# Kernel tuning notes

Hardware: AMD Instinct MI355X
Metric: run time of the kernel (lower is better)

Reference implementation:

```python
import jax, jax.numpy as jnp
import numpy as np

N_NODES = 50000
N_EDGES = 800000
D_FEAT = 96
HIDDEN = 96
AVG_DEG = 16.0


def setup_inputs() -> dict:
    key = jax.random.key(0)
    k1, k2, k3, k4, k5 = jax.random.split(key, 5)
    x = jax.random.normal(k1, (N_NODES, D_FEAT), dtype=jnp.float32)
    row = jax.random.randint(k2, (N_EDGES,), 0, N_NODES)
    col = jax.random.randint(k3, (N_EDGES,), 0, N_NODES)
    edge_index = jnp.stack([row, col]).astype(jnp.int32)  # [2, E]
    # normalized adjacency values ~ 1/degree scale
    edge_weight = jax.random.uniform(k4, (N_EDGES,), dtype=jnp.float32) / AVG_DEG
    # init_w: small normal + identity (random=False path)
    W = 0.1 * jax.random.normal(k5, (D_FEAT, HIDDEN), dtype=jnp.float32) + jnp.eye(D_FEAT, HIDDEN, dtype=jnp.float32)
    b = jnp.zeros((HIDDEN,), dtype=jnp.float32)
    return {"x": x, "W": W, "b": b, "edge_index": edge_index, "edge_weight": edge_weight}


def reference(x, W, b, edge_index, edge_weight):
    # dense projection + bias
    h = x @ W + b  # [N, H]
    # sparse adj matmul: out[i] = sum_e w_e * h[col_e] for row_e == i
    row, col = edge_index[0], edge_index[1]
    msgs = edge_weight[:, None] * h[col]  # [E, H]
    pre_nonlinearity = jax.ops.segment_sum(msgs, row, num_segments=N_NODES)  # [N, H]
    # inference path: no dropout (training=None)
    output = jax.nn.elu(pre_nonlinearity)
    return (pre_nonlinearity, output)
```

## Files before the change

### kernel.cpp

```cpp
#include <hip/hip_runtime.h>


#define D 96
#define BSHIFT 5
#define BROWS 32
#define CAP 768
#define CPAD 16
#define EB_CHUNK 3200
#define NBKT_MAX 1600
#define GR 64
#define NFRAG 18

typedef unsigned long long u64;
typedef unsigned short u16;
typedef unsigned int u32;

typedef __attribute__((ext_vector_type(8))) __bf16 bf8_t;
typedef __attribute__((ext_vector_type(8))) short s8_t;
typedef __attribute__((ext_vector_type(4))) float f4_t;

__device__ __forceinline__ u16 f2bf(float f) {
  const u32 u = __float_as_uint(f);
  return (u16)((u + 0x7FFFu + ((u >> 16) & 1u)) >> 16);
}
__device__ __forceinline__ float bf2f(u16 s) {
  return __uint_as_float(((u32)s) << 16);
}

__device__ __forceinline__ f4_t mfma16(s8_t a, s8_t b, f4_t c) {
  return __builtin_amdgcn_mfma_f32_16x16x32_bf16(
      __builtin_bit_cast(bf8_t, a), __builtin_bit_cast(bf8_t, b), c, 0, 0, 0);
}

__global__ __launch_bounds__(256) void setup_kernel(
    const float* __restrict__ W, u16* __restrict__ whi, u16* __restrict__ wlo,
    int* __restrict__ bcur, int nbkt) {
  const int i = blockIdx.x * 256 + threadIdx.x;
  if (i < nbkt) bcur[i * CPAD] = 0;
  if (i < NFRAG * 64) {
    const int f = i >> 6;
    const int lane = i & 63;
    const int n = f / 3, kt = f - 3 * n;
    const int g = lane >> 4, l15 = lane & 15;
    const int col = n * 16 + l15;
#pragma unroll
    for (int j = 0; j < 8; ++j) {
      const float w = W[(kt * 32 + 8 * g + j) * D + col];
      const u16 hb = f2bf(w);
      whi[(size_t)(f * 64 + lane) * 8 + j] = hb;
      wlo[(size_t)(f * 64 + lane) * 8 + j] = f2bf(w - bf2f(hb));
    }
  }
}

struct BzSmem {
  int cnt[NBKT_MAX];
  int cur[NBKT_MAX];
  int rbuf[EB_CHUNK];
};

__global__ __launch_bounds__(256, 6) void fused_gemm_bucketize(
    const float* __restrict__ x, const u16* __restrict__ whi,
    const u16* __restrict__ wlo, const float* __restrict__ bias,
    u16* __restrict__ h16, int n_nodes,
    const int* __restrict__ rows, const int* __restrict__ cols,
    const float* __restrict__ ew, int* __restrict__ bcur,
    u64* __restrict__ tmp, int n_edges, int nbkt, int bb) {
  __shared__ BzSmem sm;
  const int tid = threadIdx.x;

  if ((int)blockIdx.x < bb) {
    for (int i = tid; i < NBKT_MAX; i += 256) sm.cnt[i] = 0;
    __syncthreads();
    const int e0 = blockIdx.x * EB_CHUNK;
    const int e1 = min(e0 + EB_CHUNK, n_edges);
    for (int e = e0 + tid; e < e1; e += 256) {
      const int r = rows[e];
      sm.rbuf[e - e0] = r;
      atomicAdd(&sm.cnt[r >> BSHIFT], 1);
    }
    __syncthreads();
    for (int b = tid; b < nbkt; b += 256) {
      const int c = sm.cnt[b];
      sm.cur[b] = (c > 0) ? atomicAdd(&bcur[b * CPAD], c) : 0;
    }
    __syncthreads();
    for (int e = e0 + tid; e < e1; e += 256) {
      const int r = sm.rbuf[e - e0];
      const int b = r >> BSHIFT;
      const u64 u = ((u64)__float_as_uint(ew[e]) << 32) |
                    ((u64)(r & (BROWS - 1)) << 20) | (u64)(unsigned)cols[e];
      const int pos = atomicAdd(&sm.cur[b], 1);
      if (pos < CAP) tmp[(size_t)b * CAP + pos] = u;
    }
  } else {
    const int wid = tid >> 6;
    const int lane = tid & 63;
    const int l15 = lane & 15;
    const int g = lane >> 4;
    const int row0 = ((int)blockIdx.x - bb) * GR + wid * 16;

    const int ra = min(row0 + l15, n_nodes - 1);
    const float* xr = x + (size_t)ra * D;
    s8_t ah[3], al[3];
#pragma unroll
    for (int kt = 0; kt < 3; ++kt) {
      const float4 v0 = *(const float4*)(xr + kt * 32 + 8 * g);
      const float4 v1 = *(const float4*)(xr + kt * 32 + 8 * g + 4);
      const float vv[8] = {v0.x, v0.y, v0.z, v0.w, v1.x, v1.y, v1.z, v1.w};
#pragma unroll
      for (int j = 0; j < 8; ++j) {
        const u16 hb = f2bf(vv[j]);
        ah[kt][j] = (short)hb;
        al[kt][j] = (short)f2bf(vv[j] - bf2f(hb));
      }
    }

    f4_t acc[6];
#pragma unroll
    for (int n = 0; n < 6; ++n) {
      const float bv = bias[n * 16 + l15];
      acc[n][0] = bv; acc[n][1] = bv; acc[n][2] = bv; acc[n][3] = bv;
    }

#pragma unroll
    for (int kt = 0; kt < 3; ++kt) {
#pragma unroll
      for (int n = 0; n < 6; ++n) {
        const int f = n * 3 + kt;
        const s8_t bh = *(const s8_t*)(whi + (size_t)(f * 64 + lane) * 8);
        const s8_t bl = *(const s8_t*)(wlo + (size_t)(f * 64 + lane) * 8);
        acc[n] = mfma16(ah[kt], bh, acc[n]);
        acc[n] = mfma16(al[kt], bh, acc[n]);
        acc[n] = mfma16(ah[kt], bl, acc[n]);
      }
    }

#pragma unroll
    for (int n = 0; n < 6; ++n) {
#pragma unroll
      for (int r = 0; r < 4; ++r) {
        const int row = row0 + 4 * g + r;
        if (row < n_nodes)
          h16[(size_t)row * D + n * 16 + l15] = f2bf(acc[n][r]);
      }
    }
  }
}

__global__ __launch_bounds__(256) void bucket_gather_kernel(
    const int* __restrict__ bcur, const u64* __restrict__ tmp,
    const u16* __restrict__ h16, float* __restrict__ pre,
    float* __restrict__ out, int n_nodes) {
  __shared__ u64 raw[CAP];
  __shared__ u64 se[CAP];
  __shared__ int cnt[BROWS];
  __shared__ int off[BROWS + 1];
  __shared__ int cur[BROWS];
  const int tid = threadIdx.x;
  const int b = blockIdx.x;
  if (tid < BROWS) cnt[tid] = 0;
  __syncthreads();

  const int base = b * CAP;
  int count = bcur[b * CPAD];
  if (count > CAP) count = CAP;

  for (int k = tid; k < count; k += 256) {
    const u64 u = tmp[base + k];
    raw[k] = u;
    atomicAdd(&cnt[(int)((u >> 20) & (BROWS - 1))], 1);
  }
  __syncthreads();

  if (tid < BROWS) off[tid + 1] = cnt[tid];
  if (tid == 0) off[0] = 0;
  __syncthreads();
  for (int d = 1; d <= BROWS; d <<= 1) {
    int v = 0;
    if (tid <= BROWS && tid >= d) v = off[tid - d];
    __syncthreads();
    if (tid <= BROWS) off[tid] += v;
    __syncthreads();
  }
  if (tid < BROWS) cur[tid] = off[tid];
  __syncthreads();

  for (int k = tid; k < count; k += 256) {
    const u64 u = raw[k];
    const int rl = (int)((u >> 20) & (BROWS - 1));
    se[atomicAdd(&cur[rl], 1)] = u;
  }
  __syncthreads();

  const int g = tid >> 5;
  const int lane = tid & 31;
  const int row0 = b * BROWS;
#pragma unroll
  for (int j = 0; j < 4; ++j) {
    const int r = g * 4 + j;
    const int row = row0 + r;
    const int s = off[r], e = off[r + 1];
    float a0 = 0.f, a1 = 0.f, a2 = 0.f;
    int k = s;
    for (; k + 3 < e; k += 4) {
      const u64 u0 = se[k], u1 = se[k + 1], u2 = se[k + 2], u3 = se[k + 3];
      const u16* h0 = h16 + (size_t)(u0 & 0xFFFFF) * D;
      const u16* h1 = h16 + (size_t)(u1 & 0xFFFFF) * D;
      const u16* h2 = h16 + (size_t)(u2 & 0xFFFFF) * D;
      const u16* h3 = h16 + (size_t)(u3 & 0xFFFFF) * D;
      const float w0 = __uint_as_float((u32)(u0 >> 32));
      const float w1 = __uint_as_float((u32)(u1 >> 32));
      const float w2 = __uint_as_float((u32)(u2 >> 32));
      const float w3 = __uint_as_float((u32)(u3 >> 32));
      const float p00 = bf2f(h0[lane]), p01 = bf2f(h0[lane + 32]), p02 = bf2f(h0[lane + 64]);
      const float p10 = bf2f(h1[lane]), p11 = bf2f(h1[lane + 32]), p12 = bf2f(h1[lane + 64]);
      const float p20 = bf2f(h2[lane]), p21 = bf2f(h2[lane + 32]), p22 = bf2f(h2[lane + 64]);
      const float p30 = bf2f(h3[lane]), p31 = bf2f(h3[lane + 32]), p32 = bf2f(h3[lane + 64]);
      a0 = fmaf(w0, p00, a0); a1 = fmaf(w0, p01, a1); a2 = fmaf(w0, p02, a2);
      a0 = fmaf(w1, p10, a0); a1 = fmaf(w1, p11, a1); a2 = fmaf(w1, p12, a2);
      a0 = fmaf(w2, p20, a0); a1 = fmaf(w2, p21, a1); a2 = fmaf(w2, p22, a2);
      a0 = fmaf(w3, p30, a0); a1 = fmaf(w3, p31, a1); a2 = fmaf(w3, p32, a2);
    }
    for (; k < e; ++k) {
      const u64 u = se[k];
      const u16* hr = h16 + (size_t)(u & 0xFFFFF) * D;
      const float w = __uint_as_float((u32)(u >> 32));
      a0 = fmaf(w, bf2f(hr[lane]), a0);
      a1 = fmaf(w, bf2f(hr[lane + 32]), a1);
      a2 = fmaf(w, bf2f(hr[lane + 64]), a2);
    }
    if (row < n_nodes) {
      float* pr = pre + (size_t)row * D;
      float* orow = out + (size_t)row * D;
      pr[lane] = a0; pr[lane + 32] = a1; pr[lane + 64] = a2;
      orow[lane]      = a0 > 0.f ? a0 : (__expf(a0) - 1.f);
      orow[lane + 32] = a1 > 0.f ? a1 : (__expf(a1) - 1.f);
      orow[lane + 64] = a2 > 0.f ? a2 : (__expf(a2) - 1.f);
    }
  }
}

extern "C" void kernel_launch(void* const* d_in, const int* in_sizes, int n_in,
                              void* d_out, int out_size, void* d_ws, size_t ws_size,
                              hipStream_t stream) {
  const float* x  = (const float*)d_in[0];
  const float* W  = (const float*)d_in[1];
  const float* b  = (const float*)d_in[2];
  const int*   ei = (const int*)d_in[3];
  const float* ew = (const float*)d_in[4];

  const int n_nodes = in_sizes[0] / D;
  const int n_edges = in_sizes[4];
  const int* rows = ei;
  const int* cols = ei + n_edges;

  float* pre  = (float*)d_out;
  float* outp = pre + (size_t)n_nodes * D;

  const int nbkt = (n_nodes + BROWS - 1) / BROWS;

  char* ws = (char*)d_ws;
  u16*  h16  = (u16*)ws;   ws += (size_t)n_nodes * D * sizeof(u16);
  int*  bcur = (int*)ws;   ws += (size_t)nbkt * CPAD * sizeof(int);
  u64*  tmp  = (u64*)ws;   ws += (size_t)nbkt * CAP * sizeof(u64);
  u16*  whi  = (u16*)ws;   ws += (size_t)NFRAG * 64 * 8 * sizeof(u16);
  u16*  wlo  = (u16*)ws;

  setup_kernel<<<(nbkt + 255) / 256, 256, 0, stream>>>(W, whi, wlo, bcur, nbkt);

  const int gb = (n_nodes + GR - 1) / GR;
  const int bb = (n_edges + EB_CHUNK - 1) / EB_CHUNK;
  fused_gemm_bucketize<<<gb + bb, 256, 0, stream>>>(
      x, whi, wlo, b, h16, n_nodes, rows, cols, ew, bcur, tmp, n_edges, nbkt, bb);

  bucket_gather_kernel<<<nbkt, 256, 0, stream>>>(bcur, tmp, h16, pre, outp, n_nodes);
}
```

Baseline: 151.3 us.

## Replace shared-memory two-pass bucketize with direct global atomics per edge

The bucketize blocks no longer count per-bucket edges in shared memory and reserve ranges with one global atomic per bucket. Each edge now does its own global atomicAdd on the padded bucket counter and writes its packed entry directly. This removes the shared memory footprint, two block barriers and the row staging buffer, so more blocks can be resident alongside the GEMM blocks. In exchange it issues 800k global atomics, with about 16 per counter per block, which raises contention.

```diff
diff --git a/kernel.cpp b/kernel.cpp
--- a/kernel.cpp
+++ b/kernel.cpp
@@ -6,8 +6,7 @@
 #define BROWS 32
 #define CAP 768
 #define CPAD 16
-#define EB_CHUNK 3200
-#define NBKT_MAX 1600
+#define EB_CHUNK 1024
 #define GR 64
 #define NFRAG 18
 
@@ -53,44 +52,26 @@
   }
 }
 
-struct BzSmem {
-  int cnt[NBKT_MAX];
-  int cur[NBKT_MAX];
-  int rbuf[EB_CHUNK];
-};
-
-__global__ __launch_bounds__(256, 6) void fused_gemm_bucketize(
+__global__ __launch_bounds__(256) void fused_gemm_bucketize(
     const float* __restrict__ x, const u16* __restrict__ whi,
     const u16* __restrict__ wlo, const float* __restrict__ bias,
     u16* __restrict__ h16, int n_nodes,
     const int* __restrict__ rows, const int* __restrict__ cols,
     const float* __restrict__ ew, int* __restrict__ bcur,
-    u64* __restrict__ tmp, int n_edges, int nbkt, int bb) {
-  __shared__ BzSmem sm;
+    u64* __restrict__ tmp, int n_edges, int bb) {
   const int tid = threadIdx.x;
 
   if ((int)blockIdx.x < bb) {
-    for (int i = tid; i < NBKT_MAX; i += 256) sm.cnt[i] = 0;
-    __syncthreads();
     const int e0 = blockIdx.x * EB_CHUNK;
     const int e1 = min(e0 + EB_CHUNK, n_edges);
     for (int e = e0 + tid; e < e1; e += 256) {
       const int r = rows[e];
-      sm.rbuf[e - e0] = r;
-      atomicAdd(&sm.cnt[r >> BSHIFT], 1);
-    }
-    __syncthreads();
-    for (int b = tid; b < nbkt; b += 256) {
-      const int c = sm.cnt[b];
-      sm.cur[b] = (c > 0) ? atomicAdd(&bcur[b * CPAD], c) : 0;
-    }
-    __syncthreads();
-    for (int e = e0 + tid; e < e1; e += 256) {
-      const int r = sm.rbuf[e - e0];
+      const int c = cols[e];
+      const float w = ew[e];
       const int b = r >> BSHIFT;
-      const u64 u = ((u64)__float_as_uint(ew[e]) << 32) |
-                    ((u64)(r & (BROWS - 1)) << 20) | (u64)(unsigned)cols[e];
-      const int pos = atomicAdd(&sm.cur[b], 1);
+      const u64 u = ((u64)__float_as_uint(w) << 32) |
+                    ((u64)(r & (BROWS - 1)) << 20) | (u64)(unsigned)c;
+      const int pos = atomicAdd(&bcur[b * CPAD], 1);
       if (pos < CAP) tmp[(size_t)b * CAP + pos] = u;
     }
   } else {
@@ -272,7 +253,7 @@
   const int gb = (n_nodes + GR - 1) / GR;
   const int bb = (n_edges + EB_CHUNK - 1) / EB_CHUNK;
   fused_gemm_bucketize<<<gb + bb, 256, 0, stream>>>(
-      x, whi, wlo, b, h16, n_nodes, rows, cols, ew, bcur, tmp, n_edges, nbkt, bb);
+      x, whi, wlo, b, h16, n_nodes, rows, cols, ew, bcur, tmp, n_edges, bb);
 
   bucket_gather_kernel<<<nbkt, 256, 0, stream>>>(bcur, tmp, h16, pre, outp, n_nodes);
 }
```

Measured after the change: 167.5 us. 10.7% more time.
